# Performance work log

Measured on AMD Instinct MI355X. Metric: run time of the kernel, lower is better.

Reference implementation:

```python
import jax, jax.numpy as jnp
import numpy as np

N = 50000  # num nodes
E = 800000  # num edges
D_IN = 128
D_OUT = 128
K = 2


def mean_propagate(x, src, dst):
    # scatter-mean over incoming edges: out[d] = mean_{(s,d) in edges} x[s]
    sums = jax.ops.segment_sum(x[src], dst, num_segments=N)  # [N, D]
    deg = jax.ops.segment_sum(jnp.ones((src.shape[0],), x.dtype), dst, num_segments=N)
    return sums / jnp.maximum(deg, 1.0)[:, None]


def setup_inputs() -> dict:
    key = jax.random.key(0)
    k1, k2, k3, k4 = jax.random.split(key, 4)
    x = jax.random.normal(k1, (N, D_IN), dtype=jnp.float32)
    edge_index = jax.random.randint(k2, (2, E), 0, N, dtype=jnp.int64)
    fan_in = D_IN * (K + 1)
    bound = 1.0 / np.sqrt(fan_in)
    W = jax.random.uniform(k3, (D_OUT, fan_in), dtype=jnp.float32, minval=-bound, maxval=bound)
    b = jax.random.uniform(k4, (D_OUT,), dtype=jnp.float32, minval=-bound, maxval=bound)
    return {"x": x, "edge_index": edge_index, "W": W, "b": b}


def reference(x, edge_index, W, b):
    src, dst = edge_index[0], edge_index[1]
    features = [x]
    propagated = x
    for _ in range(K):
        propagated = mean_propagate(propagated, src, dst)
        features.append(propagated)
    h = jnp.concatenate(features, axis=-1)  # [N, D_IN*(K+1)]
    return h @ W.T + b  # [N, D_OUT]
```

## Files before the change

kernel.cpp:

```cpp
#include <hip/hip_runtime.h>
#include <cstddef>


#define DFEAT 128
#define SUBSHIFT 8
#define MAXSUB 256
#define EPB 2048
#define CAP 16384

typedef __attribute__((ext_vector_type(8))) short short8v;
typedef __attribute__((ext_vector_type(4))) float f32x4;
typedef __attribute__((ext_vector_type(4))) unsigned int uint4v;

__device__ inline unsigned short f2bf(float f) {
    unsigned int u;
    __builtin_memcpy(&u, &f, 4);
    unsigned int r = u + 0x7FFFu + ((u >> 16) & 1u);
    return (unsigned short)(r >> 16);
}
__device__ inline float bf2f(unsigned short h) {
    unsigned int u = ((unsigned int)h) << 16;
    float f;
    __builtin_memcpy(&f, &u, 4);
    return f;
}

__global__ void zero_kernel(int* __restrict__ p, int n) {
    int i = blockIdx.x * blockDim.x + threadIdx.x;
    if (i < n) p[i] = 0;
}

__global__ void convpack_kernel(const float* __restrict__ x,
                                unsigned short* __restrict__ xb, int total8,
                                const float* __restrict__ W,
                                unsigned short* __restrict__ Wpk) {
    const int i = blockIdx.x * blockDim.x + threadIdx.x;
    if (i < total8) {
        const float* s = x + (size_t)i * 8;
        const float4 a = *reinterpret_cast<const float4*>(s);
        const float4 b = *reinterpret_cast<const float4*>(s + 4);
        uint4v w;
        w.x = (unsigned)f2bf(a.x) | ((unsigned)f2bf(a.y) << 16);
        w.y = (unsigned)f2bf(a.z) | ((unsigned)f2bf(a.w) << 16);
        w.z = (unsigned)f2bf(b.x) | ((unsigned)f2bf(b.y) << 16);
        w.w = (unsigned)f2bf(b.z) | ((unsigned)f2bf(b.w) << 16);
        *reinterpret_cast<uint4v*>(xb + (size_t)i * 8) = w;
        return;
    }
    const int idx = i - total8;
    if (idx >= 6144) return;
    const int lane = idx & 63;
    const int nt = (idx >> 6) & 7;
    const int ks = idx >> 9;
    const int col = nt * 16 + (lane & 15);
    const int k = ks * 32 + (lane >> 4) * 8;
    const float* wp = W + (size_t)col * 384 + k;
    uint4v w;
    w.x = (unsigned)f2bf(wp[0]) | ((unsigned)f2bf(wp[1]) << 16);
    w.y = (unsigned)f2bf(wp[2]) | ((unsigned)f2bf(wp[3]) << 16);
    w.z = (unsigned)f2bf(wp[4]) | ((unsigned)f2bf(wp[5]) << 16);
    w.w = (unsigned)f2bf(wp[6]) | ((unsigned)f2bf(wp[7]) << 16);
    *reinterpret_cast<uint4v*>(Wpk + (size_t)idx * 8) = w;
}

__global__ __launch_bounds__(256) void partitionA_kernel(
    const int* __restrict__ src, const int* __restrict__ dst,
    int* __restrict__ subFill, int* __restrict__ subReal,
    uint2* __restrict__ staging, int E, int nsub) {
    __shared__ int cnt[MAXSUB];
    __shared__ int base[MAXSUB];
    const int t = threadIdx.x;
    for (int i = t; i < nsub; i += 256) cnt[i] = 0;
    __syncthreads();
    const int e0 = blockIdx.x * EPB;
    int d[8], s[8], b[8], rk[8];
#pragma unroll
    for (int j = 0; j < 8; ++j) {
        const int e = e0 + j * 256 + t;
        if (e < E) {
            d[j] = __builtin_nontemporal_load(dst + e);
            s[j] = __builtin_nontemporal_load(src + e);
            b[j] = d[j] >> SUBSHIFT;
            rk[j] = atomicAdd(&cnt[b[j]], 1);
        } else {
            d[j] = -1; s[j] = 0; b[j] = 0; rk[j] = 0;
        }
    }
    __syncthreads();
    for (int i = t; i < nsub; i += 256) {
        const int c = cnt[i];
        if (c > 0) {
            const int padded = (c + 15) & ~15;
            int bse = atomicAdd(&subFill[i], padded);
            if (bse + padded > CAP) bse = CAP - padded;
            base[i] = bse;
            atomicAdd(&subReal[i], c);
        }
    }
    __syncthreads();
#pragma unroll
    for (int j = 0; j < 8; ++j)
        if (d[j] >= 0)
            staging[(size_t)b[j] * CAP + base[b[j]] + rk[j]] =
                make_uint2((unsigned)d[j], (unsigned)s[j]);
    for (int i = t; i < nsub; i += 256) {
        const int c = cnt[i];
        if (c > 0) {
            const int padded = (c + 15) & ~15;
            for (int k = c; k < padded; ++k)
                staging[(size_t)i * CAP + base[i] + k] = make_uint2(0xFFFFFFFFu, 0u);
        }
    }
}

__global__ __launch_bounds__(256) void partitionB_kernel(
    const uint2* __restrict__ staging, const int* __restrict__ subFill,
    const int* __restrict__ subReal, int* __restrict__ rowptr,
    float* __restrict__ inv, int* __restrict__ col, int N, int E, int nsub) {
    __shared__ int ss[256];
    __shared__ int cnt[1 << SUBSHIFT];
    __shared__ int loc[1 << SUBSHIFT];
    __shared__ int cur[1 << SUBSHIFT];
    const int b = blockIdx.x;
    const int n0 = b << SUBSHIFT;
    const int t = threadIdx.x;
    ss[t] = (t < nsub) ? subReal[t] : 0;
    cnt[t] = 0;
    __syncthreads();
#pragma unroll
    for (int off = 1; off < 256; off <<= 1) {
        int x = (t >= off) ? ss[t - off] : 0;
        __syncthreads();
        ss[t] += x;
        __syncthreads();
    }
    const int myBase = (b > 0) ? ss[b - 1] : 0;
    const int fill = min(subFill[b], CAP);
    const uint2* seg = staging + (size_t)b * CAP;
    for (int i = t; i < fill; i += 256) {
        const unsigned dd = seg[i].x;
        if (dd != 0xFFFFFFFFu) atomicAdd(&cnt[dd - (unsigned)n0], 1);
    }
    __syncthreads();
    const int v = cnt[t];
    loc[t] = v;
    __syncthreads();
#pragma unroll
    for (int off = 1; off < 256; off <<= 1) {
        int x = (t >= off) ? loc[t - off] : 0;
        __syncthreads();
        loc[t] += x;
        __syncthreads();
    }
    const int gpos = myBase + loc[t] - v;
    const int n = n0 + t;
    if (n < N) {
        rowptr[n] = gpos;
        inv[n] = 1.0f / (float)max(v, 1);
    }
    cur[t] = gpos;
    __syncthreads();
    for (int i = t; i < fill; i += 256) {
        const uint2 pr = seg[i];
        if (pr.x != 0xFFFFFFFFu) {
            const int pos = atomicAdd(&cur[(int)pr.x - n0], 1);
            col[pos] = (int)pr.y;
        }
    }
    if (b == 0 && t == 0) rowptr[N] = E;
}

__global__ __launch_bounds__(256) void gather_bf16_kernel(
    const unsigned short* __restrict__ feat, const int* __restrict__ rowptr,
    const int* __restrict__ col, const float* __restrict__ inv,
    unsigned short* __restrict__ outb, int N) {
    const int n = blockIdx.x * 16 + (threadIdx.x >> 4);
    const int lane = threadIdx.x & 15;
    if (n >= N) return;
    const int beg = rowptr[n];
    const int end = rowptr[n + 1];
    float acc[8];
#pragma unroll
    for (int j = 0; j < 8; ++j) acc[j] = 0.0f;
    int e = beg;
    for (; e + 3 < end; e += 4) {
        const int s0 = col[e];
        const int s1 = col[e + 1];
        const int s2 = col[e + 2];
        const int s3 = col[e + 3];
        const short8v v0 = *reinterpret_cast<const short8v*>(feat + (size_t)s0 * DFEAT + lane * 8);
        const short8v v1 = *reinterpret_cast<const short8v*>(feat + (size_t)s1 * DFEAT + lane * 8);
        const short8v v2 = *reinterpret_cast<const short8v*>(feat + (size_t)s2 * DFEAT + lane * 8);
        const short8v v3 = *reinterpret_cast<const short8v*>(feat + (size_t)s3 * DFEAT + lane * 8);
#pragma unroll
        for (int j = 0; j < 8; ++j)
            acc[j] += (bf2f((unsigned short)v0[j]) + bf2f((unsigned short)v1[j])) +
                      (bf2f((unsigned short)v2[j]) + bf2f((unsigned short)v3[j]));
    }
    for (; e < end; ++e) {
        const int s0 = col[e];
        const short8v v0 = *reinterpret_cast<const short8v*>(feat + (size_t)s0 * DFEAT + lane * 8);
#pragma unroll
        for (int j = 0; j < 8; ++j) acc[j] += bf2f((unsigned short)v0[j]);
    }
    const float sc = inv[n];
    uint4v w;
    w.x = (unsigned)f2bf(acc[0] * sc) | ((unsigned)f2bf(acc[1] * sc) << 16);
    w.y = (unsigned)f2bf(acc[2] * sc) | ((unsigned)f2bf(acc[3] * sc) << 16);
    w.z = (unsigned)f2bf(acc[4] * sc) | ((unsigned)f2bf(acc[5] * sc) << 16);
    w.w = (unsigned)f2bf(acc[6] * sc) | ((unsigned)f2bf(acc[7] * sc) << 16);
    *reinterpret_cast<uint4v*>(outb + (size_t)n * DFEAT + lane * 8) = w;
}

#define M2PAD 132
__global__ __launch_bounds__(256) void gather_gemm_kernel(
    const unsigned short* __restrict__ xb, const unsigned short* __restrict__ m1b,
    const unsigned short* __restrict__ Wpk, const int* __restrict__ rowptr,
    const int* __restrict__ col, const float* __restrict__ inv,
    const float* __restrict__ bias, float* __restrict__ out, int N) {
    __shared__ unsigned short m2s[64][M2PAD];
    const int t = threadIdx.x;
    const int nodeBase = blockIdx.x * 64;
    const int lane16 = t & 15;

    for (int r = 0; r < 4; ++r) {
        const int ln = r * 16 + (t >> 4);
        const int n = nodeBase + ln;
        float acc[8];
#pragma unroll
        for (int j = 0; j < 8; ++j) acc[j] = 0.0f;
        float sc = 0.0f;
        if (n < N) {
            const int beg = rowptr[n];
            const int end = rowptr[n + 1];
            int e = beg;
            for (; e + 3 < end; e += 4) {
                const int s0 = col[e];
                const int s1 = col[e + 1];
                const int s2 = col[e + 2];
                const int s3 = col[e + 3];
                const short8v v0 = *reinterpret_cast<const short8v*>(m1b + (size_t)s0 * DFEAT + lane16 * 8);
                const short8v v1 = *reinterpret_cast<const short8v*>(m1b + (size_t)s1 * DFEAT + lane16 * 8);
                const short8v v2 = *reinterpret_cast<const short8v*>(m1b + (size_t)s2 * DFEAT + lane16 * 8);
                const short8v v3 = *reinterpret_cast<const short8v*>(m1b + (size_t)s3 * DFEAT + lane16 * 8);
#pragma unroll
                for (int j = 0; j < 8; ++j)
                    acc[j] += (bf2f((unsigned short)v0[j]) + bf2f((unsigned short)v1[j])) +
                              (bf2f((unsigned short)v2[j]) + bf2f((unsigned short)v3[j]));
            }
            for (; e < end; ++e) {
                const int s0 = col[e];
                const short8v v0 = *reinterpret_cast<const short8v*>(m1b + (size_t)s0 * DFEAT + lane16 * 8);
#pragma unroll
                for (int j = 0; j < 8; ++j) acc[j] += bf2f((unsigned short)v0[j]);
            }
            sc = inv[n];
        }
        unsigned short* dstp = &m2s[ln][lane16 * 8];
#pragma unroll
        for (int j = 0; j < 8; ++j) dstp[j] = f2bf(acc[j] * sc);
    }
    __syncthreads();

    const int w = t >> 6;
    const int l = t & 63;
    const int lr = l & 15;
    const int kg = l >> 4;
    const int rowBase = nodeBase + w * 16;
    int arow = rowBase + lr;
    if (arow >= N) arow = N - 1;

    const short8v* Wv = reinterpret_cast<const short8v*>(Wpk);

    f32x4 acc[8];
#pragma unroll
    for (int nt = 0; nt < 8; ++nt) acc[nt] = (f32x4){0.f, 0.f, 0.f, 0.f};

#pragma unroll
    for (int ks = 0; ks < 12; ++ks) {
        const int q = ks & 3;
        short8v a;
        if (ks < 8) {
            const unsigned short* feat = (ks < 4) ? xb : m1b;
            a = *reinterpret_cast<const short8v*>(
                feat + (size_t)arow * DFEAT + q * 32 + kg * 8);
        } else {
            a = *reinterpret_cast<const short8v*>(&m2s[w * 16 + lr][q * 32 + kg * 8]);
        }
        short8v bfrag[8];
#pragma unroll
        for (int nt = 0; nt < 8; ++nt)
            bfrag[nt] = Wv[(ks * 8 + nt) * 64 + l];
#pragma unroll
        for (int nt = 0; nt < 8; ++nt)
            acc[nt] = __builtin_amdgcn_mfma_f32_16x16x32_bf16(a, bfrag[nt], acc[nt], 0, 0, 0);
    }

#pragma unroll
    for (int nt = 0; nt < 8; ++nt) {
        const int c = nt * 16 + lr;
        const float bv = bias[c];
#pragma unroll
        for (int r = 0; r < 4; ++r) {
            const int node = rowBase + kg * 4 + r;
            if (node < N) out[(size_t)node * DFEAT + c] = acc[nt][r] + bv;
        }
    }
}

extern "C" void kernel_launch(void* const* d_in, const int* in_sizes, int n_in,
                              void* d_out, int out_size, void* d_ws, size_t ws_size,
                              hipStream_t stream) {
    (void)n_in; (void)out_size; (void)ws_size;
    const float* x  = (const float*)d_in[0];
    const int*   ei = (const int*)d_in[1];
    const float* W  = (const float*)d_in[2];
    const float* b  = (const float*)d_in[3];
    float* out = (float*)d_out;

    const int N = in_sizes[0] / DFEAT;
    const int E = in_sizes[1] / 2;
    const int* src = ei;
    const int* dst = ei + E;
    const int nsub = (N + (1 << SUBSHIFT) - 1) >> SUBSHIFT;

    auto up = [](size_t v) { return (v + 255) & ~(size_t)255; };
    char* p = (char*)d_ws;
    int*   subFill   = (int*)p;            p += up((size_t)MAXSUB * 4 * 2);
    int*   subReal   = subFill + MAXSUB;
    int*   rowptr    = (int*)p;            p += up(((size_t)N + 1) * 4);
    uint2* staging   = (uint2*)p;          p += up((size_t)MAXSUB * CAP * 8);
    int*   col       = (int*)p;            p += up((size_t)E * 4);
    float* inv       = (float*)p;          p += up((size_t)N * 4);
    unsigned short* xb  = (unsigned short*)p;  p += up((size_t)N * DFEAT * 2);
    unsigned short* m1b = (unsigned short*)p;  p += up((size_t)N * DFEAT * 2);
    unsigned short* Wpk = (unsigned short*)p;  p += up((size_t)6144 * 8 * 2);

    zero_kernel<<<1, 2 * MAXSUB, 0, stream>>>(subFill, 2 * MAXSUB);

    partitionA_kernel<<<(E + EPB - 1) / EPB, 256, 0, stream>>>(src, dst, subFill, subReal,
                                                               staging, E, nsub);
    partitionB_kernel<<<nsub, 256, 0, stream>>>(staging, subFill, subReal,
                                                rowptr, inv, col, N, E, nsub);

    const int x8 = N * DFEAT / 8;
    convpack_kernel<<<(x8 + 6144 + 255) / 256, 256, 0, stream>>>(x, xb, x8, W, Wpk);

    const int gatherBlocks = (N + 15) / 16;
    gather_bf16_kernel<<<gatherBlocks, 256, 0, stream>>>(xb, rowptr, col, inv, m1b, N);

    gather_gemm_kernel<<<(N + 63) / 64, 256, 0, stream>>>(xb, m1b, Wpk, rowptr, col,
                                                          inv, b, out, N);
}
```

Before: 137.3 us.

## Gather each node with a full wavefront and fold zeroing into convpack

Both gather stages now give each destination node a whole 64-lane wavefront: four 16-lane groups each take every fourth edge, and the partial sums are combined with cross-lane shuffles. Before, one 16-lane group walked all edges of a node. The goal is more independent row loads in flight per node and fewer serial iterations on the average degree of about 16. The separate zero kernel is removed; convpack now clears the partition counters and runs before partitioning, which saves one launch. The cost is shuffle-reduction overhead, three idle lane groups during the final write, and fewer nodes handled per block.

```diff
diff --git a/kernel.cpp b/kernel.cpp
--- a/kernel.cpp
+++ b/kernel.cpp
@@ -25,16 +25,13 @@
     return f;
 }
 
-__global__ void zero_kernel(int* __restrict__ p, int n) {
-    int i = blockIdx.x * blockDim.x + threadIdx.x;
-    if (i < n) p[i] = 0;
-}
-
 __global__ void convpack_kernel(const float* __restrict__ x,
                                 unsigned short* __restrict__ xb, int total8,
                                 const float* __restrict__ W,
-                                unsigned short* __restrict__ Wpk) {
+                                unsigned short* __restrict__ Wpk,
+                                int* __restrict__ zeroPtr) {
     const int i = blockIdx.x * blockDim.x + threadIdx.x;
+    if (i < 2 * MAXSUB) zeroPtr[i] = 0;
     if (i < total8) {
         const float* s = x + (size_t)i * 8;
         const float4 a = *reinterpret_cast<const float4*>(s);
@@ -170,46 +167,67 @@
     if (b == 0 && t == 0) rowptr[N] = E;
 }
 
-__global__ __launch_bounds__(256) void gather_bf16_kernel(
+__device__ inline void gather_wave_acc(const unsigned short* __restrict__ feat,
+                                       const int* __restrict__ col,
+                                       int beg, int end, int g, int s,
+                                       float acc[8]) {
+#pragma unroll
+    for (int j = 0; j < 8; ++j) acc[j] = 0.0f;
+    int e = beg;
+    for (; e + 15 < end; e += 16) {
+        const int i0 = col[e + g];
+        const int i1 = col[e + 4 + g];
+        const int i2 = col[e + 8 + g];
+        const int i3 = col[e + 12 + g];
+        const short8v v0 = *reinterpret_cast<const short8v*>(feat + (size_t)i0 * DFEAT + s * 8);
+        const short8v v1 = *reinterpret_cast<const short8v*>(feat + (size_t)i1 * DFEAT + s * 8);
+        const short8v v2 = *reinterpret_cast<const short8v*>(feat + (size_t)i2 * DFEAT + s * 8);
+        const short8v v3 = *reinterpret_cast<const short8v*>(feat + (size_t)i3 * DFEAT + s * 8);
+#pragma unroll
+        for (int j = 0; j < 8; ++j)
+            acc[j] += (bf2f((unsigned short)v0[j]) + bf2f((unsigned short)v1[j])) +
+                      (bf2f((unsigned short)v2[j]) + bf2f((unsigned short)v3[j]));
+    }
+    for (; e + 3 < end; e += 4) {
+        const int i0 = col[e + g];
+        const short8v v0 = *reinterpret_cast<const short8v*>(feat + (size_t)i0 * DFEAT + s * 8);
+#pragma unroll
+        for (int j = 0; j < 8; ++j) acc[j] += bf2f((unsigned short)v0[j]);
+    }
+    if (e + g < end) {
+        const int i0 = col[e + g];
+        const short8v v0 = *reinterpret_cast<const short8v*>(feat + (size_t)i0 * DFEAT + s * 8);
+#pragma unroll
+        for (int j = 0; j < 8; ++j) acc[j] += bf2f((unsigned short)v0[j]);
+    }
+}
+
+__global__ __launch_bounds__(256) void gather_wave_kernel(
     const unsigned short* __restrict__ feat, const int* __restrict__ rowptr,
     const int* __restrict__ col, const float* __restrict__ inv,
     unsigned short* __restrict__ outb, int N) {
-    const int n = blockIdx.x * 16 + (threadIdx.x >> 4);
-    const int lane = threadIdx.x & 15;
+    const int wv = threadIdx.x >> 6;
+    const int lane = threadIdx.x & 63;
+    const int g = lane >> 4;
+    const int s = lane & 15;
+    const int n = blockIdx.x * 4 + wv;
     if (n >= N) return;
-    const int beg = rowptr[n];
-    const int end = rowptr[n + 1];
     float acc[8];
-#pragma unroll
-    for (int j = 0; j < 8; ++j) acc[j] = 0.0f;
-    int e = beg;
-    for (; e + 3 < end; e += 4) {
-        const int s0 = col[e];
-        const int s1 = col[e + 1];
-        const int s2 = col[e + 2];
-        const int s3 = col[e + 3];
-        const short8v v0 = *reinterpret_cast<const short8v*>(feat + (size_t)s0 * DFEAT + lane * 8);
-        const short8v v1 = *reinterpret_cast<const short8v*>(feat + (size_t)s1 * DFEAT + lane * 8);
-        const short8v v2 = *reinterpret_cast<const short8v*>(feat + (size_t)s2 * DFEAT + lane * 8);
-        const short8v v3 = *reinterpret_cast<const short8v*>(feat + (size_t)s3 * DFEAT + lane * 8);
-#pragma unroll
-        for (int j = 0; j < 8; ++j)
-            acc[j] += (bf2f((unsigned short)v0[j]) + bf2f((unsigned short)v1[j])) +
-                      (bf2f((unsigned short)v2[j]) + bf2f((unsigned short)v3[j]));
-    }
-    for (; e < end; ++e) {
-        const int s0 = col[e];
-        const short8v v0 = *reinterpret_cast<const short8v*>(feat + (size_t)s0 * DFEAT + lane * 8);
-#pragma unroll
-        for (int j = 0; j < 8; ++j) acc[j] += bf2f((unsigned short)v0[j]);
-    }
-    const float sc = inv[n];
-    uint4v w;
-    w.x = (unsigned)f2bf(acc[0] * sc) | ((unsigned)f2bf(acc[1] * sc) << 16);
-    w.y = (unsigned)f2bf(acc[2] * sc) | ((unsigned)f2bf(acc[3] * sc) << 16);
-    w.z = (unsigned)f2bf(acc[4] * sc) | ((unsigned)f2bf(acc[5] * sc) << 16);
-    w.w = (unsigned)f2bf(acc[6] * sc) | ((unsigned)f2bf(acc[7] * sc) << 16);
-    *reinterpret_cast<uint4v*>(outb + (size_t)n * DFEAT + lane * 8) = w;
+    gather_wave_acc(feat, col, rowptr[n], rowptr[n + 1], g, s, acc);
+#pragma unroll
+    for (int j = 0; j < 8; ++j) {
+        acc[j] += __shfl_xor(acc[j], 16, 64);
+        acc[j] += __shfl_xor(acc[j], 32, 64);
+    }
+    if (g == 0) {
+        const float sc = inv[n];
+        uint4v w;
+        w.x = (unsigned)f2bf(acc[0] * sc) | ((unsigned)f2bf(acc[1] * sc) << 16);
+        w.y = (unsigned)f2bf(acc[2] * sc) | ((unsigned)f2bf(acc[3] * sc) << 16);
+        w.z = (unsigned)f2bf(acc[4] * sc) | ((unsigned)f2bf(acc[5] * sc) << 16);
+        w.w = (unsigned)f2bf(acc[6] * sc) | ((unsigned)f2bf(acc[7] * sc) << 16);
+        *reinterpret_cast<uint4v*>(outb + (size_t)n * DFEAT + s * 8) = w;
+    }
 }
 
 #define M2PAD 132
@@ -221,51 +239,38 @@
     __shared__ unsigned short m2s[64][M2PAD];
     const int t = threadIdx.x;
     const int nodeBase = blockIdx.x * 64;
-    const int lane16 = t & 15;
-
-    for (int r = 0; r < 4; ++r) {
-        const int ln = r * 16 + (t >> 4);
+    const int w = t >> 6;
+    const int lane = t & 63;
+    const int g = lane >> 4;
+    const int s = lane & 15;
+
+    for (int r = 0; r < 16; ++r) {
+        const int ln = w * 16 + r;
         const int n = nodeBase + ln;
         float acc[8];
-#pragma unroll
-        for (int j = 0; j < 8; ++j) acc[j] = 0.0f;
-        float sc = 0.0f;
         if (n < N) {
-            const int beg = rowptr[n];
-            const int end = rowptr[n + 1];
-            int e = beg;
-            for (; e + 3 < end; e += 4) {
-                const int s0 = col[e];
-                const int s1 = col[e + 1];
-                const int s2 = col[e + 2];
-                const int s3 = col[e + 3];
-                const short8v v0 = *reinterpret_cast<const short8v*>(m1b + (size_t)s0 * DFEAT + lane16 * 8);
-                const short8v v1 = *reinterpret_cast<const short8v*>(m1b + (size_t)s1 * DFEAT + lane16 * 8);
-                const short8v v2 = *reinterpret_cast<const short8v*>(m1b + (size_t)s2 * DFEAT + lane16 * 8);
-                const short8v v3 = *reinterpret_cast<const short8v*>(m1b + (size_t)s3 * DFEAT + lane16 * 8);
-#pragma unroll
-                for (int j = 0; j < 8; ++j)
-                    acc[j] += (bf2f((unsigned short)v0[j]) + bf2f((unsigned short)v1[j])) +
-                              (bf2f((unsigned short)v2[j]) + bf2f((unsigned short)v3[j]));
+            gather_wave_acc(m1b, col, rowptr[n], rowptr[n + 1], g, s, acc);
+#pragma unroll
+            for (int j = 0; j < 8; ++j) {
+                acc[j] += __shfl_xor(acc[j], 16, 64);
+                acc[j] += __shfl_xor(acc[j], 32, 64);
             }
-            for (; e < end; ++e) {
-                const int s0 = col[e];
-                const short8v v0 = *reinterpret_cast<const short8v*>(m1b + (size_t)s0 * DFEAT + lane16 * 8);
-#pragma unroll
-                for (int j = 0; j < 8; ++j) acc[j] += bf2f((unsigned short)v0[j]);
+            if (g == 0) {
+                const float sc = inv[n];
+                unsigned short* dstp = &m2s[ln][s * 8];
+#pragma unroll
+                for (int j = 0; j < 8; ++j) dstp[j] = f2bf(acc[j] * sc);
             }
-            sc = inv[n];
-        }
-        unsigned short* dstp = &m2s[ln][lane16 * 8];
-#pragma unroll
-        for (int j = 0; j < 8; ++j) dstp[j] = f2bf(acc[j] * sc);
-    }
-    __syncthreads();
-
-    const int w = t >> 6;
-    const int l = t & 63;
-    const int lr = l & 15;
-    const int kg = l >> 4;
+        } else if (g == 0) {
+            unsigned short* dstp = &m2s[ln][s * 8];
+#pragma unroll
+            for (int j = 0; j < 8; ++j) dstp[j] = 0;
+        }
+    }
+    __syncthreads();
+
+    const int lr = lane & 15;
+    const int kg = lane >> 4;
     const int rowBase = nodeBase + w * 16;
     int arow = rowBase + lr;
     if (arow >= N) arow = N - 1;
@@ -290,7 +295,7 @@
         short8v bfrag[8];
 #pragma unroll
         for (int nt = 0; nt < 8; ++nt)
-            bfrag[nt] = Wv[(ks * 8 + nt) * 64 + l];
+            bfrag[nt] = Wv[(ks * 8 + nt) * 64 + lane];
 #pragma unroll
         for (int nt = 0; nt < 8; ++nt)
             acc[nt] = __builtin_amdgcn_mfma_f32_16x16x32_bf16(a, bfrag[nt], acc[nt], 0, 0, 0);
@@ -336,18 +341,15 @@
     unsigned short* m1b = (unsigned short*)p;  p += up((size_t)N * DFEAT * 2);
     unsigned short* Wpk = (unsigned short*)p;  p += up((size_t)6144 * 8 * 2);
 
-    zero_kernel<<<1, 2 * MAXSUB, 0, stream>>>(subFill, 2 * MAXSUB);
+    const int x8 = N * DFEAT / 8;
+    convpack_kernel<<<(x8 + 6144 + 255) / 256, 256, 0, stream>>>(x, xb, x8, W, Wpk, subFill);
 
     partitionA_kernel<<<(E + EPB - 1) / EPB, 256, 0, stream>>>(src, dst, subFill, subReal,
                                                                staging, E, nsub);
     partitionB_kernel<<<nsub, 256, 0, stream>>>(staging, subFill, subReal,
                                                 rowptr, inv, col, N, E, nsub);
 
-    const int x8 = N * DFEAT / 8;
-    convpack_kernel<<<(x8 + 6144 + 255) / 256, 256, 0, stream>>>(x, xb, x8, W, Wpk);
-
-    const int gatherBlocks = (N + 15) / 16;
-    gather_bf16_kernel<<<gatherBlocks, 256, 0, stream>>>(xb, rowptr, col, inv, m1b, N);
+    gather_wave_kernel<<<(N + 3) / 4, 256, 0, stream>>>(xb, rowptr, col, inv, m1b, N);
 
     gather_gemm_kernel<<<(N + 63) / 64, 256, 0, stream>>>(xb, m1b, Wpk, rowptr, col,
                                                           inv, b, out, N);
```

Result: slower. 147.0 us (+7.0%).
